# Performance work log

Measured on AMD Instinct MI355X. Metric: run time of the kernel, lower is better.

Reference implementation:

```python
import jax, jax.numpy as jnp
import numpy as np

DIM = 192
HEADS = 6
H = 64
W = 64
B = 16
HID = int(DIM * 4.0)


def make_rope(Hh, Ww, c):
    # mirrors torch RoPE buffer: k_max = c // (2*2), angles (H,W,c//2)
    k_max = c // 4
    theta = 1.0 / (10000.0 ** (np.arange(k_max) / k_max))
    hi = np.arange(Hh)[:, None, None] * theta  # (H,1,k)
    wi = np.arange(Ww)[None, :, None] * theta  # (1,W,k)
    angles = np.concatenate([np.broadcast_to(hi, (Hh, Ww, k_max)),
                             np.broadcast_to(wi, (Hh, Ww, k_max))], axis=-1)
    return jnp.asarray(np.cos(angles), jnp.float32), jnp.asarray(np.sin(angles), jnp.float32)


def rope_apply(x, cos, sin):
    # x: (b,H,W,c); complex multiply on (re,im) pairs along last dim
    b, Hh, Ww, c = x.shape
    xr = x.reshape(b, Hh, Ww, c // 2, 2)
    re, im = xr[..., 0], xr[..., 1]
    out = jnp.stack([re * cos - im * sin, re * sin + im * cos], axis=-1)
    return out.reshape(b, Hh, Ww, c)


def dwconv(x, w, b):
    # depthwise 3x3, NCHW, kernel (C,1,3,3)
    C = x.shape[1]
    y = jax.lax.conv_general_dilated(x, w, (1, 1), 'SAME',
                                     dimension_numbers=('NCHW', 'OIHW', 'NCHW'),
                                     feature_group_count=C)
    return y + b[None, :, None, None]


def conv1x1(x, w, b):
    return jnp.einsum('bchw,oc->bohw', x, w) + b[None, :, None, None]


def ln2d(x, w, b):
    # LayerNorm over channel dim at each spatial location
    mu = x.mean(axis=1, keepdims=True)
    var = x.var(axis=1, keepdims=True)
    xn = (x - mu) / jnp.sqrt(var + 1e-5)
    return xn * w[None, :, None, None] + b[None, :, None, None]


def setup_inputs() -> dict:
    key = jax.random.key(0)
    ks = jax.random.split(key, 32)
    s = 0.02
    def p(i, shape):
        return jax.random.normal(ks[i], shape, jnp.float32) * s
    return {
        'x': jax.random.normal(ks[0], (B, DIM, H, W), jnp.float32),
        'cpe1_w': p(1, (DIM, 1, 3, 3)), 'cpe1_b': p(2, (DIM,)),
        'norm1_w': jnp.ones((DIM,), jnp.float32), 'norm1_b': jnp.zeros((DIM,), jnp.float32),
        'act_proj_w': p(3, (DIM, DIM)), 'act_proj_b': p(4, (DIM,)),
        'in_proj_w': p(5, (DIM, DIM)), 'in_proj_b': p(6, (DIM,)),
        'dwc_w': p(7, (DIM, 1, 3, 3)), 'dwc_b': p(8, (DIM,)),
        'qk_w': p(9, (2 * DIM, DIM)), 'qk_b': p(10, (2 * DIM,)),
        'lepe_w': p(11, (DIM, 1, 3, 3)), 'lepe_b': p(12, (DIM,)),
        'out_proj_w': p(13, (DIM, DIM)), 'out_proj_b': p(14, (DIM,)),
        'cpe2_w': p(15, (DIM, 1, 3, 3)), 'cpe2_b': p(16, (DIM,)),
        'norm2_w': jnp.ones((DIM,), jnp.float32), 'norm2_b': jnp.zeros((DIM,), jnp.float32),
        'fc1_w': p(17, (HID, DIM)), 'fc1_b': p(18, (HID,)),
        'fc2_w': p(19, (DIM, HID)), 'fc2_b': p(20, (DIM,)),
    }


def reference(x, cpe1_w, cpe1_b, norm1_w, norm1_b, act_proj_w, act_proj_b,
              in_proj_w, in_proj_b, dwc_w, dwc_b, qk_w, qk_b, lepe_w, lepe_b,
              out_proj_w, out_proj_b, cpe2_w, cpe2_b, norm2_w, norm2_b,
              fc1_w, fc1_b, fc2_w, fc2_b):
    b, c, Hh, Ww = x.shape
    n = Hh * Ww
    d = c // HEADS
    cos, sin = make_rope(Hh, Ww, c)

    # x = x + cpe1(x)
    x = x + dwconv(x, cpe1_w, cpe1_b)

    # MLLA block on norm1(x)
    y = ln2d(x, norm1_w, norm1_b)
    act_res = jax.nn.silu(conv1x1(y, act_proj_w, act_proj_b))
    y = conv1x1(y, in_proj_w, in_proj_b)
    t = jax.nn.silu(dwconv(y, dwc_w, dwc_b)).transpose(0, 2, 3, 1).reshape(b, n, c)

    # linear attention with ELU+1 feature map, RoPE, LePE
    qk = t @ qk_w.T + qk_b
    q = jax.nn.elu(qk[..., :c]) + 1.0
    k = jax.nn.elu(qk[..., c:]) + 1.0
    v = t
    q_rope = rope_apply(q.reshape(b, Hh, Ww, c), cos, sin).reshape(b, n, HEADS, d).transpose(0, 2, 1, 3)
    k_rope = rope_apply(k.reshape(b, Hh, Ww, c), cos, sin).reshape(b, n, HEADS, d).transpose(0, 2, 1, 3)
    qh = q.reshape(b, n, HEADS, d).transpose(0, 2, 1, 3)
    kh = k.reshape(b, n, HEADS, d).transpose(0, 2, 1, 3)
    vh = v.reshape(b, n, HEADS, d).transpose(0, 2, 1, 3)
    kmean = kh.mean(axis=2, keepdims=True)  # (b,h,1,d)
    z = 1.0 / (jnp.einsum('bhnd,bhmd->bhnm', qh, kmean) + 1e-6)  # (b,h,n,1)
    scale = n ** -0.5
    kv = jnp.einsum('bhnd,bhne->bhde', k_rope * scale, vh * scale)  # (b,h,d,d)
    attn = jnp.einsum('bhnd,bhde->bhne', q_rope, kv) * z  # (b,h,n,d)
    attn = attn.transpose(0, 2, 1, 3).reshape(b, n, c)
    v_img = vh.transpose(0, 2, 1, 3).reshape(b, Hh, Ww, c).transpose(0, 3, 1, 2)
    lepe = dwconv(v_img, lepe_w, lepe_b).transpose(0, 2, 3, 1).reshape(b, n, c)
    attn = attn + lepe

    y = attn.transpose(0, 2, 1).reshape(b, c, Hh, Ww)
    y = conv1x1(y * act_res, out_proj_w, out_proj_b)
    x = x + y

    # x = x + cpe2(x)
    x = x + dwconv(x, cpe2_w, cpe2_b)

    # MLP on norm2(x)
    y = ln2d(x, norm2_w, norm2_b)
    y = conv1x1(y, fc1_w, fc1_b)
    y = jax.nn.gelu(y, approximate=False)
    y = conv1x1(y, fc2_w, fc2_b)
    return x + y
```

## Files before the change

### kernel.cpp

```cpp
#include <hip/hip_runtime.h>
#include <hip/hip_bf16.h>

#define BQ 16
#define CH 192
#define HH 64
#define WW 64
#define HWSZ 4096
#define NPIX 65536
#define NHEADS 6
#define HDIM 32
#define NPAIR 96
#define KMAXR 48
#define HID 768

typedef __hip_bfloat16 bf16;
typedef __attribute__((ext_vector_type(8))) short short8;
typedef __attribute__((ext_vector_type(4))) float floatx4;

static __device__ __forceinline__ float b2f(bf16 v) { return __bfloat162float(v); }
static __device__ __forceinline__ bf16 f2b(float v) { return __float2bfloat16(v); }

static __device__ __forceinline__ float4 ld4(const float* p) { return *(const float4*)p; }
static __device__ __forceinline__ float4 ld4(const bf16* p) {
  uint2 u = *(const uint2*)p;
  return make_float4(__uint_as_float(u.x << 16), __uint_as_float(u.x & 0xffff0000u),
                     __uint_as_float(u.y << 16), __uint_as_float(u.y & 0xffff0000u));
}

template <int ACT>
static __device__ __forceinline__ float actf(float v) {
  if (ACT == 1) return v / (1.f + expf(-v));
  if (ACT == 2) return (v > 0.f) ? v + 1.f : expf(v);
  if (ACT == 3) return 0.5f * v * (1.f + erff(v * 0.70710678118654752f));
  return v;
}
static __device__ __forceinline__ void stv(float* p, float v) { *p = v; }
static __device__ __forceinline__ void stv(bf16* p, float v) { *p = __float2bfloat16(v); }

__global__ __launch_bounds__(256) void k_transpose_in(const float* __restrict__ in,
                                                      float* __restrict__ out) {
  __shared__ float tile[32][33];
  int c0 = blockIdx.x * 32, hw0 = blockIdx.y * 32, b = blockIdx.z;
  int tx = threadIdx.x, ty = threadIdx.y;
  const float* src = in + (size_t)b * CH * HWSZ;
  #pragma unroll
  for (int j = 0; j < 32; j += 8)
    tile[ty + j][tx] = src[(size_t)(c0 + ty + j) * HWSZ + hw0 + tx];
  __syncthreads();
  float* dst = out + (size_t)b * HWSZ * CH;
  #pragma unroll
  for (int j = 0; j < 32; j += 8)
    dst[(size_t)(hw0 + ty + j) * CH + c0 + tx] = tile[tx][ty + j];
}

__global__ __launch_bounds__(256) void k_transpose_out(const float* __restrict__ in,
                                                       float* __restrict__ out) {
  __shared__ float tile[32][33];
  int c0 = blockIdx.x * 32, hw0 = blockIdx.y * 32, b = blockIdx.z;
  int tx = threadIdx.x, ty = threadIdx.y;
  const float* src = in + (size_t)b * HWSZ * CH;
  #pragma unroll
  for (int j = 0; j < 32; j += 8)
    tile[ty + j][tx] = src[(size_t)(hw0 + ty + j) * CH + c0 + tx];
  __syncthreads();
  float* dst = out + (size_t)b * CH * HWSZ;
  #pragma unroll
  for (int j = 0; j < 32; j += 8)
    dst[(size_t)(c0 + ty + j) * HWSZ + hw0 + tx] = tile[tx][ty + j];
}

__global__ __launch_bounds__(256) void k_rope(float* __restrict__ cosT, float* __restrict__ sinT) {
  int i = blockIdx.x * 256 + threadIdx.x;
  if (i >= NPAIR * HWSZ) return;
  int hw = i & (HWSZ - 1);
  int p = i >> 12;
  int h = hw >> 6, w = hw & 63;
  int j = (p < KMAXR) ? p : p - KMAXR;
  float theta = powf(10000.f, -(float)j / (float)KMAXR);
  float pos = (p < KMAXR) ? (float)h : (float)w;
  float ang = pos * theta;
  cosT[i] = cosf(ang);
  sinT[i] = sinf(ang);
}

#define WTOT 479232
__global__ __launch_bounds__(256) void k_wcvt(const float* __restrict__ ap,
                                              const float* __restrict__ ip,
                                              const float* __restrict__ qk,
                                              const float* __restrict__ op,
                                              const float* __restrict__ f1,
                                              const float* __restrict__ f2,
                                              bf16* __restrict__ o) {
  int i = (blockIdx.x * 256 + threadIdx.x) * 4;
  if (i >= WTOT) return;
  const float* src;
  int off;
  if (i < 36864)       { src = ap; off = 0; }
  else if (i < 73728)  { src = ip; off = 36864; }
  else if (i < 147456) { src = qk; off = 73728; }
  else if (i < 184320) { src = op; off = 147456; }
  else if (i < 331776) { src = f1; off = 184320; }
  else                 { src = f2; off = 331776; }
  float4 v = ld4(src + (i - off));
  __align__(8) bf16 t4[4] = {f2b(v.x), f2b(v.y), f2b(v.z), f2b(v.w)};
  *(uint2*)&o[i] = *(uint2*)t4;
}

template <typename TI>
__global__ __launch_bounds__(192) void k_cpe_ln(const TI* __restrict__ in,
                                                const float* __restrict__ w,
                                                const float* __restrict__ bias,
                                                const float* __restrict__ g,
                                                const float* __restrict__ bt,
                                                float* __restrict__ x1o,
                                                bf16* __restrict__ yo) {
  __shared__ float grs[12][4], grq[12][4];
  int t = threadIdx.x;
  int cg = t % 48, st = t / 48;
  int c0 = cg * 4;
  int gpix = blockIdx.x * 16 + st * 4;
  int hw = gpix & (HWSZ - 1);
  int h = hw >> 6, wx = hw & 63;
  float4 w4[9];
  #pragma unroll
  for (int i = 0; i < 9; i++) w4[i] = ld4(w + c0 * 9 + i * 4);
  const float* wf = (const float*)w4;
  float4 bi = ld4(bias + c0);
  float4 acc[4];
  #pragma unroll
  for (int i = 0; i < 4; i++) acc[i] = bi;
  const TI* base = in + (size_t)gpix * CH + c0;
  #pragma unroll
  for (int dh = -1; dh <= 1; dh++) {
    bool rv = ((unsigned)(h + dh) < HH);
    float4 tap[6];
    #pragma unroll
    for (int c = 0; c < 6; c++) {
      int col = wx - 1 + c;
      bool v = rv && ((unsigned)col < WW);
      tap[c] = v ? ld4(base + (dh * WW + (c - 1)) * CH) : make_float4(0, 0, 0, 0);
    }
    #pragma unroll
    for (int i = 0; i < 4; i++) {
      #pragma unroll
      for (int dw = 0; dw < 3; dw++) {
        const int tp = (dh + 1) * 3 + dw;
        float4 tv = tap[i + dw];
        acc[i].x += tv.x * wf[0 * 9 + tp];
        acc[i].y += tv.y * wf[1 * 9 + tp];
        acc[i].z += tv.z * wf[2 * 9 + tp];
        acc[i].w += tv.w * wf[3 * 9 + tp];
      }
      if (dh == 0) {
        acc[i].x += tap[i + 1].x;
        acc[i].y += tap[i + 1].y;
        acc[i].z += tap[i + 1].z;
        acc[i].w += tap[i + 1].w;
      }
    }
  }
  float s4[4], q4[4];
  #pragma unroll
  for (int i = 0; i < 4; i++) {
    *(float4*)&x1o[(size_t)(gpix + i) * CH + c0] = acc[i];
    s4[i] = acc[i].x + acc[i].y + acc[i].z + acc[i].w;
    q4[i] = acc[i].x * acc[i].x + acc[i].y * acc[i].y + acc[i].z * acc[i].z +
            acc[i].w * acc[i].w;
  }
  #pragma unroll
  for (int m = 1; m <= 8; m <<= 1) {
    #pragma unroll
    for (int i = 0; i < 4; i++) {
      s4[i] += __shfl_xor(s4[i], m, 64);
      q4[i] += __shfl_xor(q4[i], m, 64);
    }
  }
  if ((t & 15) == 0) {
    #pragma unroll
    for (int i = 0; i < 4; i++) { grs[t >> 4][i] = s4[i]; grq[t >> 4][i] = q4[i]; }
  }
  __syncthreads();
  int s3 = st * 3;
  float4 gg = ld4(g + c0);
  float4 bb = ld4(bt + c0);
  #pragma unroll
  for (int i = 0; i < 4; i++) {
    float S = grs[s3][i] + grs[s3 + 1][i] + grs[s3 + 2][i];
    float SS = grq[s3][i] + grq[s3 + 1][i] + grq[s3 + 2][i];
    float mu = S * (1.f / CH);
    float inv = rsqrtf(SS * (1.f / CH) - mu * mu + 1e-5f);
    __align__(8) bf16 tmp[4] = {f2b((acc[i].x - mu) * inv * gg.x + bb.x),
                                f2b((acc[i].y - mu) * inv * gg.y + bb.y),
                                f2b((acc[i].z - mu) * inv * gg.z + bb.z),
                                f2b((acc[i].w - mu) * inv * gg.w + bb.w)};
    *(uint2*)&yo[(size_t)(gpix + i) * CH + c0] = *(uint2*)tmp;
  }
}

template <int MODE>
__global__ __launch_bounds__(192) void k_dwconv_strip(const bf16* __restrict__ in,
                                                      const float* __restrict__ w,
                                                      const float* __restrict__ bias,
                                                      bf16* __restrict__ out) {
  int t = threadIdx.x;
  int cg = t % 48, st = t / 48;
  int c0 = cg * 4;
  int gpix = blockIdx.x * 16 + st * 4;
  int hw = gpix & (HWSZ - 1);
  int h = hw >> 6, wx = hw & 63;
  float4 w4[9];
  #pragma unroll
  for (int i = 0; i < 9; i++) w4[i] = ld4(w + c0 * 9 + i * 4);
  const float* wf = (const float*)w4;
  float4 bi = ld4(bias + c0);
  float4 acc[4];
  #pragma unroll
  for (int i = 0; i < 4; i++) acc[i] = bi;
  const bf16* base = in + (size_t)gpix * CH + c0;
  #pragma unroll
  for (int dh = -1; dh <= 1; dh++) {
    bool rv = ((unsigned)(h + dh) < HH);
    float4 tap[6];
    #pragma unroll
    for (int c = 0; c < 6; c++) {
      int col = wx - 1 + c;
      bool v = rv && ((unsigned)col < WW);
      tap[c] = v ? ld4(base + (dh * WW + (c - 1)) * CH) : make_float4(0, 0, 0, 0);
    }
    #pragma unroll
    for (int i = 0; i < 4; i++) {
      #pragma unroll
      for (int dw = 0; dw < 3; dw++) {
        const int tp = (dh + 1) * 3 + dw;
        float4 tv = tap[i + dw];
        acc[i].x += tv.x * wf[0 * 9 + tp];
        acc[i].y += tv.y * wf[1 * 9 + tp];
        acc[i].z += tv.z * wf[2 * 9 + tp];
        acc[i].w += tv.w * wf[3 * 9 + tp];
      }
    }
  }
  #pragma unroll
  for (int i = 0; i < 4; i++) {
    bf16* op = out + (size_t)(gpix + i) * CH + c0;
    float a0 = acc[i].x, a1 = acc[i].y, a2 = acc[i].z, a3 = acc[i].w;
    if (MODE == 1) {
      a0 = a0 / (1.f + expf(-a0));
      a1 = a1 / (1.f + expf(-a1));
      a2 = a2 / (1.f + expf(-a2));
      a3 = a3 / (1.f + expf(-a3));
    } else {
      float4 cur = ld4(op);
      a0 += cur.x; a1 += cur.y; a2 += cur.z; a3 += cur.w;
    }
    __align__(8) bf16 tmp[4] = {f2b(a0), f2b(a1), f2b(a2), f2b(a3)};
    *(uint2*)op = *(uint2*)tmp;
  }
}

template <int ACT, int MULA, int RES, typename TO>
__global__ __launch_bounds__(256) void k_gemm(const bf16* __restrict__ A,
                                              const bf16* __restrict__ A2,
                                              const bf16* __restrict__ Wt,
                                              const float* __restrict__ bias,
                                              const float* __restrict__ Rsd,
                                              TO* __restrict__ Cout,
                                              int M, int N, int K) {
  __shared__ bf16 As[128][72];
  __shared__ bf16 Bs[64][72];
  int t = threadIdx.x;
  int wave = t >> 6, lane = t & 63;
  int quad = lane >> 4, l16 = lane & 15;
  int m0 = blockIdx.x * 128, n0 = blockIdx.y * 64;
  floatx4 acc[2][4] = {};
  for (int kc = 0; kc < K; kc += 64) {
    #pragma unroll
    for (int i = 0; i < 4; i++) {
      int idx = t + i * 256;
      int m = idx >> 3, ck = (idx & 7) * 8;
      const bf16* pa = &A[(size_t)(m0 + m) * K + kc + ck];
      if (!MULA) {
        *(short8*)&As[m][ck] = *(const short8*)pa;
      } else {
        const bf16* pb = &A2[(size_t)(m0 + m) * K + kc + ck];
        __align__(16) bf16 tmp[8];
        #pragma unroll
        for (int j = 0; j < 8; j++) tmp[j] = f2b(b2f(pa[j]) * b2f(pb[j]));
        *(short8*)&As[m][ck] = *(const short8*)tmp;
      }
    }
    #pragma unroll
    for (int i = 0; i < 2; i++) {
      int idx = t + i * 256;
      int n = idx >> 3, ck = (idx & 7) * 8;
      *(short8*)&Bs[n][ck] = *(const short8*)&Wt[(size_t)(n0 + n) * K + kc + ck];
    }
    __syncthreads();
    #pragma unroll
    for (int ks = 0; ks < 2; ks++) {
      short8 af[2], bfr[4];
      #pragma unroll
      for (int i = 0; i < 2; i++)
        af[i] = *(const short8*)&As[wave * 32 + i * 16 + l16][ks * 32 + quad * 8];
      #pragma unroll
      for (int j = 0; j < 4; j++)
        bfr[j] = *(const short8*)&Bs[j * 16 + l16][ks * 32 + quad * 8];
      #pragma unroll
      for (int i = 0; i < 2; i++)
        #pragma unroll
        for (int j = 0; j < 4; j++)
          acc[i][j] = __builtin_amdgcn_mfma_f32_16x16x32_bf16(af[i], bfr[j], acc[i][j], 0, 0, 0);
    }
    __syncthreads();
  }
  #pragma unroll
  for (int i = 0; i < 2; i++) {
    #pragma unroll
    for (int j = 0; j < 4; j++) {
      int n = n0 + j * 16 + l16;
      float bn = bias[n];
      #pragma unroll
      for (int r = 0; r < 4; r++) {
        int m = m0 + wave * 32 + i * 16 + quad * 4 + r;
        float v = actf<ACT>(acc[i][j][r] + bn);
        if (RES) v += Rsd[(size_t)m * N + n];
        stv(&Cout[(size_t)m * N + n], v);
      }
    }
  }
}

template <int ACTA, int ACTB, int KMEAN>
__global__ __launch_bounds__(256) void k_gemm_dual(const bf16* __restrict__ A,
                                                   const bf16* __restrict__ WtA,
                                                   const float* __restrict__ biasA,
                                                   const bf16* __restrict__ WtB,
                                                   const float* __restrict__ biasB,
                                                   bf16* __restrict__ OutA,
                                                   bf16* __restrict__ OutB,
                                                   float* __restrict__ KM,
                                                   int K) {
  __shared__ bf16 As[128][72];
  __shared__ bf16 Bs[64][72];
  __shared__ float colsum[64];
  int t = threadIdx.x;
  int wave = t >> 6, lane = t & 63;
  int quad = lane >> 4, l16 = lane & 15;
  int m0 = blockIdx.x * 128, n0 = blockIdx.y * 64;
  int half = n0 >= 192;
  int n0l = half ? n0 - 192 : n0;
  const bf16* Wt = half ? WtB : WtA;
  const float* bias = half ? biasB : biasA;
  bf16* Out = half ? OutB : OutA;
  if (KMEAN && half && t < 64) colsum[t] = 0.f;
  floatx4 acc[2][4] = {};
  for (int kc = 0; kc < CH; kc += 64) {
    #pragma unroll
    for (int i = 0; i < 4; i++) {
      int idx = t + i * 256;
      int m = idx >> 3, ck = (idx & 7) * 8;
      *(short8*)&As[m][ck] = *(const short8*)&A[(size_t)(m0 + m) * CH + kc + ck];
    }
    #pragma unroll
    for (int i = 0; i < 2; i++) {
      int idx = t + i * 256;
      int n = idx >> 3, ck = (idx & 7) * 8;
      *(short8*)&Bs[n][ck] = *(const short8*)&Wt[(size_t)(n0l + n) * CH + kc + ck];
    }
    __syncthreads();
    #pragma unroll
    for (int ks = 0; ks < 2; ks++) {
      short8 af[2], bfr[4];
      #pragma unroll
      for (int i = 0; i < 2; i++)
        af[i] = *(const short8*)&As[wave * 32 + i * 16 + l16][ks * 32 + quad * 8];
      #pragma unroll
      for (int j = 0; j < 4; j++)
        bfr[j] = *(const short8*)&Bs[j * 16 + l16][ks * 32 + quad * 8];
      #pragma unroll
      for (int i = 0; i < 2; i++)
        #pragma unroll
        for (int j = 0; j < 4; j++)
          acc[i][j] = __builtin_amdgcn_mfma_f32_16x16x32_bf16(af[i], bfr[j], acc[i][j], 0, 0, 0);
    }
    __syncthreads();
  }
  #pragma unroll
  for (int j = 0; j < 4; j++) {
    int nl = n0l + j * 16 + l16;
    float bn = bias[nl];
    float csum = 0.f;
    #pragma unroll
    for (int i = 0; i < 2; i++) {
      #pragma unroll
      for (int r = 0; r < 4; r++) {
        int m = m0 + wave * 32 + i * 16 + quad * 4 + r;
        float v = half ? actf<ACTB>(acc[i][j][r] + bn) : actf<ACTA>(acc[i][j][r] + bn);
        if (KMEAN && half) csum += v;
        Out[(size_t)m * CH + nl] = f2b(v);
      }
    }
    if (KMEAN && half) atomicAdd(&colsum[j * 16 + l16], csum);
  }
  if (KMEAN && half) {
    __syncthreads();
    if (t < 64) {
      int b = m0 >> 12;
      atomicAdd(&KM[b * CH + n0l + t], colsum[t] * (1.f / 4096.f));
    }
  }
}

__global__ __launch_bounds__(256) void k_kv(const bf16* __restrict__ k,
                                            const bf16* __restrict__ v,
                                            const float* __restrict__ cosT,
                                            const float* __restrict__ sinT,
                                            float* __restrict__ kv) {
  int bh = blockIdx.x;
  int b = bh / NHEADS, hd = bh % NHEADS;
  int chunk0 = blockIdx.y * 512;
  __shared__ __align__(16) bf16 kst[32][280];
  __shared__ __align__(16) bf16 vst[32][280];
  int t = threadIdx.x;
  int wave = t >> 6, lane = t & 63;
  int quad = lane >> 4, l16 = lane & 15;
  int dh = wave >> 1, eh = wave & 1;
  floatx4 acc = {};
  for (int sub = 0; sub < 2; sub++) {
    int n0 = chunk0 + sub * 256;
    #pragma unroll
    for (int it = 0; it < 4; it++) {
      int idx = t + it * 256;
      int row = idx >> 2, c0 = (idx & 3) * 8;
      int n = n0 + row;
      size_t gi = ((size_t)(b * HWSZ + n)) * CH + hd * HDIM + c0;
      short8 vv = *(const short8*)&v[gi];
      #pragma unroll
      for (int j = 0; j < 8; j++) vst[c0 + j][row] = ((const bf16*)&vv)[j];
      float4 klo = ld4(&k[gi]);
      float4 khi = ld4(&k[gi + 4]);
      int prb = hd * 16 + (c0 >> 1);
      float cs0 = cosT[(size_t)(prb + 0) * HWSZ + n];
      float sn0 = sinT[(size_t)(prb + 0) * HWSZ + n];
      float cs1 = cosT[(size_t)(prb + 1) * HWSZ + n];
      float sn1 = sinT[(size_t)(prb + 1) * HWSZ + n];
      float cs2 = cosT[(size_t)(prb + 2) * HWSZ + n];
      float sn2 = sinT[(size_t)(prb + 2) * HWSZ + n];
      float cs3 = cosT[(size_t)(prb + 3) * HWSZ + n];
      float sn3 = sinT[(size_t)(prb + 3) * HWSZ + n];
      kst[c0 + 0][row] = f2b(klo.x * cs0 - klo.y * sn0);
      kst[c0 + 1][row] = f2b(klo.x * sn0 + klo.y * cs0);
      kst[c0 + 2][row] = f2b(klo.z * cs1 - klo.w * sn1);
      kst[c0 + 3][row] = f2b(klo.z * sn1 + klo.w * cs1);
      kst[c0 + 4][row] = f2b(khi.x * cs2 - khi.y * sn2);
      kst[c0 + 5][row] = f2b(khi.x * sn2 + khi.y * cs2);
      kst[c0 + 6][row] = f2b(khi.z * cs3 - khi.w * sn3);
      kst[c0 + 7][row] = f2b(khi.z * sn3 + khi.w * cs3);
    }
    __syncthreads();
    #pragma unroll
    for (int ks = 0; ks < 8; ks++) {
      short8 af = *(const short8*)&kst[dh * 16 + l16][ks * 32 + quad * 8];
      short8 bfr = *(const short8*)&vst[eh * 16 + l16][ks * 32 + quad * 8];
      acc = __builtin_amdgcn_mfma_f32_16x16x32_bf16(af, bfr, acc, 0, 0, 0);
    }
    __syncthreads();
  }
  int d = dh * 16 + quad * 4;
  int e = eh * 16 + l16;
  float* dst = kv + (size_t)bh * (HDIM * HDIM) + (size_t)d * HDIM + e;
  const float sc = 1.f / 4096.f;
  #pragma unroll
  for (int r = 0; r < 4; r++) atomicAdd(dst + r * HDIM, acc[r] * sc);
}

__global__ __launch_bounds__(256) void k_attn(const bf16* __restrict__ q,
                                              const float* __restrict__ kv,
                                              const float* __restrict__ kmean,
                                              const float* __restrict__ cosT,
                                              const float* __restrict__ sinT,
                                              bf16* __restrict__ attn) {
  int hd = blockIdx.y, b = blockIdx.z;
  int t = threadIdx.x;
  int hw = blockIdx.x * 256 + t;
  int bh = b * NHEADS + hd;
  __shared__ __align__(16) bf16 As[256][40];
  __shared__ __align__(16) bf16 Bs[32][40];
  int wave = t >> 6, lane = t & 63;
  int quad = lane >> 4, l16 = lane & 15;
  {
    int e = t >> 3, d0 = (t & 7) * 4;
    const float* kvp = kv + (size_t)bh * 1024;
    __align__(8) bf16 tmp[4] = {f2b(kvp[(d0 + 0) * 32 + e]), f2b(kvp[(d0 + 1) * 32 + e]),
                                f2b(kvp[(d0 + 2) * 32 + e]), f2b(kvp[(d0 + 3) * 32 + e])};
    *(uint2*)&Bs[e][d0] = *(uint2*)tmp;
  }
  int pix = b * HWSZ + hw;
  const bf16* qp = q + (size_t)pix * CH + hd * HDIM;
  float qv[32];
  #pragma unroll
  for (int i = 0; i < 32; i++) qv[i] = b2f(qp[i]);
  const float* km = kmean + b * CH + hd * HDIM;
  float z = 1e-6f;
  #pragma unroll
  for (int d = 0; d < 32; d++) z += qv[d] * km[d];
  float zi = 1.f / z;
  __align__(16) bf16 ar[32];
  #pragma unroll
  for (int p = 0; p < 16; p++) {
    float cs = cosT[(size_t)(hd * 16 + p) * HWSZ + hw];
    float sn = sinT[(size_t)(hd * 16 + p) * HWSZ + hw];
    float re = qv[2 * p], im = qv[2 * p + 1];
    ar[2 * p] = f2b(re * cs - im * sn);
    ar[2 * p + 1] = f2b(re * sn + im * cs);
  }
  #pragma unroll
  for (int i = 0; i < 4; i++) *(short8*)&As[t][i * 8] = *(const short8*)&ar[i * 8];
  __syncthreads();
  short8 af[4], bfr[2];
  #pragma unroll
  for (int nt = 0; nt < 2; nt++) bfr[nt] = *(const short8*)&Bs[nt * 16 + l16][quad * 8];
  #pragma unroll
  for (int mt = 0; mt < 4; mt++)
    af[mt] = *(const short8*)&As[wave * 64 + mt * 16 + l16][quad * 8];
  floatx4 acc[4][2] = {};
  #pragma unroll
  for (int mt = 0; mt < 4; mt++)
    #pragma unroll
    for (int nt = 0; nt < 2; nt++)
      acc[mt][nt] = __builtin_amdgcn_mfma_f32_16x16x32_bf16(af[mt], bfr[nt], acc[mt][nt], 0, 0, 0);
  __syncthreads();
  #pragma unroll
  for (int mt = 0; mt < 4; mt++)
    #pragma unroll
    for (int nt = 0; nt < 2; nt++) {
      int row = wave * 64 + mt * 16 + quad * 4;
      int col = nt * 16 + l16;
      #pragma unroll
      for (int r = 0; r < 4; r++) As[row + r][col] = f2b(acc[mt][nt][r]);
    }
  __syncthreads();
  bf16* op = attn + (size_t)pix * CH + hd * HDIM;
  #pragma unroll
  for (int i = 0; i < 4; i++) {
    short8 vv = *(const short8*)&As[t][i * 8];
    __align__(16) bf16 tmp[8];
    #pragma unroll
    for (int j = 0; j < 8; j++) tmp[j] = f2b(b2f(((const bf16*)&vv)[j]) * zi);
    *(short8*)&op[i * 8] = *(const short8*)tmp;
  }
}

extern "C" void kernel_launch(void* const* d_in, const int* in_sizes, int n_in,
                              void* d_out, int out_size, void* d_ws, size_t ws_size,
                              hipStream_t stream) {
  const float* x = (const float*)d_in[0];
  const float* cpe1w = (const float*)d_in[1];
  const float* cpe1b = (const float*)d_in[2];
  const float* n1w = (const float*)d_in[3];
  const float* n1b = (const float*)d_in[4];
  const float* apw = (const float*)d_in[5];
  const float* apb = (const float*)d_in[6];
  const float* ipw = (const float*)d_in[7];
  const float* ipb = (const float*)d_in[8];
  const float* dwcw = (const float*)d_in[9];
  const float* dwcb = (const float*)d_in[10];
  const float* qkw = (const float*)d_in[11];
  const float* qkb = (const float*)d_in[12];
  const float* lepw = (const float*)d_in[13];
  const float* lepb = (const float*)d_in[14];
  const float* opw = (const float*)d_in[15];
  const float* opb = (const float*)d_in[16];
  const float* cpe2w = (const float*)d_in[17];
  const float* cpe2b = (const float*)d_in[18];
  const float* n2w = (const float*)d_in[19];
  const float* n2b = (const float*)d_in[20];
  const float* f1w = (const float*)d_in[21];
  const float* f1b = (const float*)d_in[22];
  const float* f2w = (const float*)d_in[23];
  const float* f2b = (const float*)d_in[24];
  float* out = (float*)d_out;

  float* ws = (float*)d_ws;
  const size_t S = (size_t)NPIX * CH;
  float* FA = ws;
  float* FB = ws + S;
  bf16* barena = (bf16*)(ws + 2 * S);
  bf16* b0 = barena;
  bf16* b1 = barena + S;
  bf16* b2 = barena + 2 * S;
  bf16* KB = (bf16*)FA;
  float* COS = ws + 2 * S + 3 * S / 2;
  float* SIN = COS + (size_t)NPAIR * HWSZ;
  float* KV = SIN + (size_t)NPAIR * HWSZ;
  float* KM = KV + BQ * NHEADS * HDIM * HDIM;
  bf16* WB = (bf16*)(KM + BQ * CH);
  bf16* apw16 = WB;
  bf16* ipw16 = WB + 36864;
  bf16* qkw16 = WB + 73728;
  bf16* opw16 = WB + 147456;
  bf16* f1w16 = WB + 184320;
  bf16* f2w16 = WB + 331776;
  bf16* HIDB = (bf16*)FB;

  dim3 tb(32, 8);
  k_wcvt<<<dim3((WTOT / 4 + 255) / 256), dim3(256), 0, stream>>>(
      apw, ipw, qkw, opw, f1w, f2w, WB);
  k_transpose_in<<<dim3(6, 128, BQ), tb, 0, stream>>>(x, FA);
  k_rope<<<dim3(NPAIR * HWSZ / 256), dim3(256), 0, stream>>>(COS, SIN);
  k_cpe_ln<float><<<dim3(NPIX / 16), dim3(192), 0, stream>>>(FA, cpe1w, cpe1b, n1w, n1b, FB, b0);
  k_gemm_dual<1, 0, 0><<<dim3(NPIX / 128, 6), dim3(256), 0, stream>>>(
      b0, apw16, apb, ipw16, ipb, b1, b2, nullptr, CH);
  k_dwconv_strip<1><<<dim3(NPIX / 16), dim3(192), 0, stream>>>(b2, dwcw, dwcb, b0);
  hipMemsetAsync(KM, 0, (size_t)BQ * CH * sizeof(float), stream);
  k_gemm_dual<2, 2, 1><<<dim3(NPIX / 128, 6), dim3(256), 0, stream>>>(
      b0, qkw16, qkb, qkw16 + CH * CH, qkb + CH, b2, KB, KM, CH);
  hipMemsetAsync(KV, 0, (size_t)BQ * NHEADS * HDIM * HDIM * sizeof(float), stream);
  k_kv<<<dim3(BQ * NHEADS, 8), dim3(256), 0, stream>>>(KB, b0, COS, SIN, KV);
  k_attn<<<dim3(HWSZ / 256, NHEADS, BQ), dim3(256), 0, stream>>>(b2, KV, KM, COS, SIN, KB);
  k_dwconv_strip<2><<<dim3(NPIX / 16), dim3(192), 0, stream>>>(b0, lepw, lepb, KB);
  k_gemm<0, 1, 1, bf16><<<dim3(NPIX / 128, 3), dim3(256), 0, stream>>>(
      KB, b1, opw16, opb, FB, b2, NPIX, CH, CH);
  k_cpe_ln<bf16><<<dim3(NPIX / 16), dim3(192), 0, stream>>>(b2, cpe2w, cpe2b, n2w, n2b, FA, b0);
  for (int s = 0; s < 2; s++) {
    size_t off = (size_t)s * (NPIX / 2) * CH;
    k_gemm<3, 0, 0, bf16><<<dim3((NPIX / 2) / 128, HID / 64), dim3(256), 0, stream>>>(
        b0 + off, (const bf16*)nullptr, f1w16, f1b, (const float*)nullptr, HIDB, NPIX / 2, HID, CH);
    k_gemm<0, 0, 1, float><<<dim3((NPIX / 2) / 128, 3), dim3(256), 0, stream>>>(
        HIDB, (const bf16*)nullptr, f2w16, f2b, FA + off, FA + off, NPIX / 2, CH, HID);
  }
  k_transpose_out<<<dim3(6, 128, BQ), tb, 0, stream>>>(FA, out);
}
```

Baseline: 580.3 us.

## Fuse MLP fc1, GELU and fc2 into a single kernel with on-chip hidden

Replaces the two-pass MLP (fc1 GEMM writing a bf16 hidden buffer, then fc2 GEMM reading it) with one kernel. Each block takes 128 pixels, computes the hidden activations in 64-wide chunks, applies exact GELU into shared memory, and accumulates fc2 into registers before adding the residual. This removes the round trip of the 65536x768 hidden tensor through global memory and cuts the launch count. The cost is a 2x12 floatx4 accumulator per thread, which raises register pressure, and only 512 blocks with large LDS use, so occupancy is lower. The weight loads are also unpipelined and re-read per block.

```diff
diff --git a/kernel.cpp b/kernel.cpp
--- a/kernel.cpp
+++ b/kernel.cpp
@@ -407,6 +407,108 @@
     if (t < 64) {
       int b = m0 >> 12;
       atomicAdd(&KM[b * CH + n0l + t], colsum[t] * (1.f / 4096.f));
+    }
+  }
+}
+
+__global__ __launch_bounds__(256) void k_mlp(const bf16* __restrict__ Y,
+                                             const bf16* __restrict__ W1,
+                                             const float* __restrict__ B1,
+                                             const bf16* __restrict__ W2,
+                                             const float* __restrict__ B2,
+                                             float* __restrict__ XR) {
+  __shared__ bf16 As[128][72];
+  __shared__ bf16 Bs[192][72];
+  __shared__ bf16 Hs[128][80];
+  int t = threadIdx.x;
+  int wave = t >> 6, lane = t & 63;
+  int quad = lane >> 4, l16 = lane & 15;
+  int m0 = blockIdx.x * 128;
+  floatx4 acc2[2][12] = {};
+  for (int hc = 0; hc < 12; hc++) {
+    int h0 = hc * 64;
+    floatx4 acc1[2][4] = {};
+    for (int ks3 = 0; ks3 < 3; ks3++) {
+      int kc = ks3 * 64;
+      #pragma unroll
+      for (int i = 0; i < 4; i++) {
+        int idx = t + i * 256;
+        int m = idx >> 3, ck = (idx & 7) * 8;
+        *(short8*)&As[m][ck] = *(const short8*)&Y[(size_t)(m0 + m) * CH + kc + ck];
+      }
+      #pragma unroll
+      for (int i = 0; i < 2; i++) {
+        int idx = t + i * 256;
+        int n = idx >> 3, ck = (idx & 7) * 8;
+        *(short8*)&Bs[n][ck] = *(const short8*)&W1[(size_t)(h0 + n) * CH + kc + ck];
+      }
+      __syncthreads();
+      #pragma unroll
+      for (int ks = 0; ks < 2; ks++) {
+        short8 af[2], bfr[4];
+        #pragma unroll
+        for (int i = 0; i < 2; i++)
+          af[i] = *(const short8*)&As[wave * 32 + i * 16 + l16][ks * 32 + quad * 8];
+        #pragma unroll
+        for (int j = 0; j < 4; j++)
+          bfr[j] = *(const short8*)&Bs[j * 16 + l16][ks * 32 + quad * 8];
+        #pragma unroll
+        for (int i = 0; i < 2; i++)
+          #pragma unroll
+          for (int j = 0; j < 4; j++)
+            acc1[i][j] = __builtin_amdgcn_mfma_f32_16x16x32_bf16(af[i], bfr[j], acc1[i][j], 0, 0, 0);
+      }
+      __syncthreads();
+    }
+    #pragma unroll
+    for (int j = 0; j < 4; j++) {
+      int col = j * 16 + l16;
+      float bn = B1[h0 + col];
+      #pragma unroll
+      for (int i = 0; i < 2; i++) {
+        #pragma unroll
+        for (int r = 0; r < 4; r++) {
+          int row = wave * 32 + i * 16 + quad * 4 + r;
+          float v = acc1[i][j][r] + bn;
+          Hs[row][col] = f2b(0.5f * v * (1.f + erff(v * 0.70710678118654752f)));
+        }
+      }
+    }
+    #pragma unroll
+    for (int i = 0; i < 6; i++) {
+      int idx = t + i * 256;
+      int n = idx >> 3, ck = (idx & 7) * 8;
+      *(short8*)&Bs[n][ck] = *(const short8*)&W2[(size_t)n * HID + h0 + ck];
+    }
+    __syncthreads();
+    #pragma unroll
+    for (int ks = 0; ks < 2; ks++) {
+      short8 af[2];
+      #pragma unroll
+      for (int i = 0; i < 2; i++)
+        af[i] = *(const short8*)&Hs[wave * 32 + i * 16 + l16][ks * 32 + quad * 8];
+      #pragma unroll
+      for (int j = 0; j < 12; j++) {
+        short8 bfr = *(const short8*)&Bs[j * 16 + l16][ks * 32 + quad * 8];
+        #pragma unroll
+        for (int i = 0; i < 2; i++)
+          acc2[i][j] = __builtin_amdgcn_mfma_f32_16x16x32_bf16(af[i], bfr, acc2[i][j], 0, 0, 0);
+      }
+    }
+    __syncthreads();
+  }
+  #pragma unroll
+  for (int j = 0; j < 12; j++) {
+    int n = j * 16 + l16;
+    float bn = B2[n];
+    #pragma unroll
+    for (int i = 0; i < 2; i++) {
+      #pragma unroll
+      for (int r = 0; r < 4; r++) {
+        int m = m0 + wave * 32 + i * 16 + quad * 4 + r;
+        float* p = &XR[(size_t)m * CH + n];
+        *p = acc2[i][j][r] + bn + *p;
+      }
     }
   }
 }
@@ -601,7 +703,6 @@
   bf16* opw16 = WB + 147456;
   bf16* f1w16 = WB + 184320;
   bf16* f2w16 = WB + 331776;
-  bf16* HIDB = (bf16*)FB;
 
   dim3 tb(32, 8);
   k_wcvt<<<dim3((WTOT / 4 + 255) / 256), dim3(256), 0, stream>>>(
@@ -622,12 +723,6 @@
   k_gemm<0, 1, 1, bf16><<<dim3(NPIX / 128, 3), dim3(256), 0, stream>>>(
       KB, b1, opw16, opb, FB, b2, NPIX, CH, CH);
   k_cpe_ln<bf16><<<dim3(NPIX / 16), dim3(192), 0, stream>>>(b2, cpe2w, cpe2b, n2w, n2b, FA, b0);
-  for (int s = 0; s < 2; s++) {
-    size_t off = (size_t)s * (NPIX / 2) * CH;
-    k_gemm<3, 0, 0, bf16><<<dim3((NPIX / 2) / 128, HID / 64), dim3(256), 0, stream>>>(
-        b0 + off, (const bf16*)nullptr, f1w16, f1b, (const float*)nullptr, HIDB, NPIX / 2, HID, CH);
-    k_gemm<0, 0, 1, float><<<dim3((NPIX / 2) / 128, 3), dim3(256), 0, stream>>>(
-        HIDB, (const bf16*)nullptr, f2w16, f2b, FA + off, FA + off, NPIX / 2, CH, HID);
-  }
+  k_mlp<<<dim3(NPIX / 128), dim3(256), 0, stream>>>(b0, f1w16, f1b, f2w16, f2b, FA);
   k_transpose_out<<<dim3(6, 128, BQ), tb, 0, stream>>>(FA, out);
 }
```

Measured after the change: 629.1 us. 8.4% more time.
